# Optimization experiments

Hardware: AMD Instinct MI355X
Metric: run time of the kernel (lower is better)

## Reference

```python
import jax, jax.numpy as jnp
import numpy as np

N = 50000      # nodes
NE = 10000     # hyperedges
NNZ = 600000   # incidence pairs
DIN = 128
DOUT = 128
ALPHA_RES = 0.5  # module's residual mixing coefficient


def _glorot(key, shape):
    fan_in, fan_out = shape[1], shape[0]
    lim = float(np.sqrt(6.0 / (fan_in + fan_out)))
    return jax.random.uniform(key, shape, jnp.float32, -lim, lim)


def setup_inputs() -> dict:
    key = jax.random.key(0)
    ks = jax.random.split(key, 9)
    X = jax.random.normal(ks[0], (N, DIN), jnp.float32)
    X0 = jax.random.normal(ks[1], (N, DIN), jnp.float32)
    vertex = jax.random.randint(ks[2], (NNZ,), 0, N)
    edges = jax.random.randint(ks[3], (NNZ,), 0, NE)
    alpha = jax.random.uniform(ks[4], (NNZ,), jnp.float32)
    # single-layer MLPs -> plain Linear weights (out, in) + bias
    W1_w = _glorot(ks[5], (DOUT, DIN))
    W1_b = jnp.zeros((DOUT,), jnp.float32)
    W2_w = _glorot(ks[6], (DOUT, DIN + DOUT))
    W2_b = jnp.zeros((DOUT,), jnp.float32)
    W_w = _glorot(ks[7], (DOUT, DOUT))
    W_b = jnp.zeros((DOUT,), jnp.float32)
    return {"X": X, "vertex": vertex, "edges": edges, "X0": X0, "alpha": alpha,
            "W1_w": W1_w, "W1_b": W1_b, "W2_w": W2_w, "W2_b": W2_b,
            "W_w": W_w, "W_b": W_b}


def reference(X, vertex, edges, X0, alpha, W1_w, W1_b, W2_w, W2_b, W_w, W_b):
    a = alpha[:, None]                                   # [nnz,1]
    # vertex -> edge: gather W1(X) rows, weight, scatter-add over hyperedges
    Xw1 = X @ W1_w.T + W1_b                              # [N, dout]
    Xve = Xw1[vertex] * a                                # [nnz, dout]
    Xe = jax.ops.segment_sum(Xve, edges, num_segments=NE)  # [NE, dout]
    # edge -> vertex: gather edge feats, concat with raw vertex feats, W2, scatter-add
    Xev = jnp.concatenate([X[vertex], Xe[edges]], axis=-1)  # [nnz, din+dout]
    Xev = (Xev @ W2_w.T + W2_b) * a                      # [nnz, dout]
    Xv = jax.ops.segment_sum(Xev, vertex, num_segments=N)  # [N, dout]
    Xr = (1.0 - ALPHA_RES) * Xv + ALPHA_RES * X0         # residual mix
    return Xr @ W_w.T + W_b
```

## Files before the change

### kernel.cpp

```cpp
#include <hip/hip_runtime.h>

#define NV   50000
#define NEV  10000
#define NNZV 600000
#define DIM  128

#define NBKE 157
#define NBKV 196
#define CHUNK 4096
#define SCAP 7680

#define BPACK_OFF 0
#define WT1_OFF   24576
#define BA_OFF    40960
#define A_OFF     41216
#define B_OFF     91264
#define T_OFF     101312
#define XEBF_OFF  1381312
#define BCNTE_OFF 2021312
#define BOFFE_OFF 2021568
#define BCNTV_OFF 2021824
#define BOFFV_OFF 2022080
#define OFFE_OFF  2031328
#define CURE_OFF  2041344
#define OFFV_OFF  2101376
#define CURV_OFF  2151392
#define PV_OFF    2201920
#define PE_OUT_FLOAT_OFF 3200000

typedef __attribute__((ext_vector_type(8))) short bf16x8;
typedef __attribute__((ext_vector_type(4))) float f32x4;

__device__ __forceinline__ unsigned short f2bf(float x){
  unsigned u = __float_as_uint(x);
  u += 0x7fffu + ((u >> 16) & 1u);
  return (unsigned short)(u >> 16);
}
__device__ __forceinline__ float bf2f(unsigned short h){
  return __uint_as_float((unsigned)h << 16);
}

__global__ __launch_bounds__(128) void prep_weights(
        const float* __restrict__ W1w, const float* __restrict__ W2w,
        const float* __restrict__ W2b, const float* __restrict__ Ww,
        float* __restrict__ ws){
  int b = blockIdx.x, o = threadIdx.x;
  if (b < 384){
    float s;
    if (b < 256){
      float acc = 0.f;
      for (int m = 0; m < 128; ++m) acc += Ww[o*128 + m] * W2w[m*256 + b];
      s = 0.5f * acc;
    } else {
      s = 0.5f * Ww[o*128 + (b - 256)];
    }
    int ks = b >> 5, g = (b >> 3) & 3, j = b & 7;
    int ct = o >> 4, lo = o & 15;
    unsigned short* Bp = (unsigned short*)(ws + BPACK_OFF);
    Bp[((size_t)((ks*8 + ct)*64 + g*16 + lo))*8 + j] = f2bf(s);
  } else if (b < 512){
    int k = b - 384;
    ws[WT1_OFF + k*128 + o] = W1w[o*128 + k];
  } else {
    float acc = 0.f;
    for (int m = 0; m < 128; ++m) acc += Ww[o*128 + m] * W2b[m];
    ws[BA_OFF + o] = 0.5f * acc;
  }
}

__global__ __launch_bounds__(256) void count_bucket(
        const int* __restrict__ vertex, const int* __restrict__ edges,
        int* __restrict__ bcntE, int* __restrict__ bcntV){
  __shared__ int hE[256], hV[256];
  int t = threadIdx.x;
  hE[t] = 0; hV[t] = 0;
  __syncthreads();
  int i0 = blockIdx.x * 2048;
  #pragma unroll
  for (int r = 0; r < 8; ++r){
    int i = i0 + r*256 + t;
    if (i < NNZV){
      atomicAdd(&hE[edges[i]  >> 6], 1);
      atomicAdd(&hV[vertex[i] >> 8], 1);
    }
  }
  __syncthreads();
  if (hE[t]) atomicAdd(bcntE + t, hE[t]);
  if (hV[t]) atomicAdd(bcntV + t, hV[t]);
}

__global__ __launch_bounds__(256) void to_bf16(
        const float* __restrict__ src, unsigned short* __restrict__ dst, int n8){
  int i = blockIdx.x*256 + threadIdx.x;
  if (i >= n8) return;
  float4 v0 = ((const float4*)src)[(size_t)i*2];
  float4 v1 = ((const float4*)src)[(size_t)i*2 + 1];
  ushort4 h0, h1;
  h0.x=f2bf(v0.x); h0.y=f2bf(v0.y); h0.z=f2bf(v0.z); h0.w=f2bf(v0.w);
  h1.x=f2bf(v1.x); h1.y=f2bf(v1.y); h1.z=f2bf(v1.z); h1.w=f2bf(v1.w);
  ((ushort4*)dst)[(size_t)i*2]     = h0;
  ((ushort4*)dst)[(size_t)i*2 + 1] = h1;
}

__global__ __launch_bounds__(256) void scan_buckets(
        const int* __restrict__ bcntE, const int* __restrict__ bcntV,
        int* __restrict__ bOffE, int* __restrict__ bOffV,
        int* __restrict__ bcurE, int* __restrict__ bcurV,
        int* __restrict__ offE, int* __restrict__ offV){
  __shared__ int s[256];
  int t = threadIdx.x;
  int c = (t < NBKE) ? bcntE[t] : 0;
  s[t] = c; __syncthreads();
  for (int d = 1; d < 256; d <<= 1){
    int x = (t >= d) ? s[t-d] : 0;
    __syncthreads(); s[t] += x; __syncthreads();
  }
  if (t < NBKE){ bOffE[t] = s[t] - c; bcurE[t] = s[t] - c; }
  if (t == 0){ bOffE[NBKE] = NNZV; offE[NEV] = NNZV; }
  __syncthreads();
  int c2 = (t < NBKV) ? bcntV[t] : 0;
  s[t] = c2; __syncthreads();
  for (int d = 1; d < 256; d <<= 1){
    int x = (t >= d) ? s[t-d] : 0;
    __syncthreads(); s[t] += x; __syncthreads();
  }
  if (t < NBKV){ bOffV[t] = s[t] - c2; bcurV[t] = s[t] - c2; }
  if (t == 0){ bOffV[NBKV] = NNZV; offV[NV] = NNZV; }
}

__global__ __launch_bounds__(256) void fill_binned(
        const int* __restrict__ vertex, const int* __restrict__ edges,
        const float* __restrict__ alpha,
        int* __restrict__ bcur, int2* __restrict__ pairs,
        int isE, int nbk){
  __shared__ int hist[256], lofs[256], gbase[256], pos[256], ss[256];
  __shared__ int2 stage[CHUNK];
  int t = threadIdx.x;
  int i0 = blockIdx.x * CHUNK;
  if (t < nbk) hist[t] = 0;
  __syncthreads();
  int pk[16], pa[16], kb[16];
  #pragma unroll
  for (int r = 0; r < 16; ++r){
    int i = i0 + r*256 + t;
    int b = -1, packed = 0, ab = 0;
    if (i < NNZV){
      int v = vertex[i], e = edges[i];
      ab = __float_as_int(alpha[i]);
      packed = isE ? ((e << 16) | v) : ((v << 14) | e);
      b = packed >> 22;
      atomicAdd(&hist[b], 1);
    }
    pk[r] = packed; pa[r] = ab; kb[r] = b;
  }
  __syncthreads();
  int c = (t < nbk) ? hist[t] : 0;
  ss[t] = c; __syncthreads();
  for (int d = 1; d < 256; d <<= 1){
    int x = (t >= d) ? ss[t-d] : 0;
    __syncthreads(); ss[t] += x; __syncthreads();
  }
  if (t < nbk){ lofs[t] = ss[t] - c; pos[t] = ss[t] - c; }
  __syncthreads();
  #pragma unroll
  for (int r = 0; r < 16; ++r){
    if (kb[r] >= 0){
      int p = atomicAdd(&pos[kb[r]], 1);
      stage[p] = make_int2(pk[r], pa[r]);
    }
  }
  __syncthreads();
  if (t < nbk){
    int cnt = hist[t];
    gbase[t] = cnt ? atomicAdd(&bcur[t], cnt) : 0;
  }
  __syncthreads();
  int total = (i0 + CHUNK <= NNZV) ? CHUNK : (NNZV - i0);
  for (int s = t; s < total; s += 256){
    int lo = 0, hi = nbk - 1;
    while (lo < hi){ int mid = (lo + hi + 1) >> 1; if (lofs[mid] <= s) lo = mid; else hi = mid - 1; }
    pairs[gbase[lo] + (s - lofs[lo])] = stage[s];
  }
}

__global__ __launch_bounds__(256) void sort_bucket(
        int2* __restrict__ pairs, const int* __restrict__ bOff,
        int* __restrict__ off, int2* __restrict__ bounce,
        int kpb, int shift, int nkeys){
  int b = blockIdx.x, t = threadIdx.x;
  int k0 = b * kpb;
  int r0 = bOff[b], r1 = bOff[b+1];
  int m = r1 - r0;
  __shared__ int hist[256], rnk[256], ssc[256];
  __shared__ int2 srt[SCAP];
  for (int q = t; q < kpb; q += 256) hist[q] = 0;
  __syncthreads();
  int px[30], py[30];
  #pragma unroll
  for (int r = 0; r < 30; ++r){
    int s = r*256 + t;
    int x = -1, y = 0;
    if (s < m && m <= SCAP){
      int2 p = pairs[r0 + s];
      x = p.x; y = p.y;
      atomicAdd(&hist[(x >> shift) - k0], 1);
    }
    px[r] = x; py[r] = y;
  }
  if (m > SCAP){
    for (int s = t; s < m; s += 256){
      int2 p = pairs[r0 + s];
      bounce[s] = p;
      atomicAdd(&hist[(p.x >> shift) - k0], 1);
    }
  }
  __syncthreads();
  int c = (t < kpb) ? hist[t] : 0;
  ssc[t] = c; __syncthreads();
  for (int d = 1; d < 256; d <<= 1){
    int x = (t >= d) ? ssc[t-d] : 0;
    __syncthreads(); ssc[t] += x; __syncthreads();
  }
  if (t < kpb){
    rnk[t] = ssc[t] - c;
    int k = k0 + t;
    if (k < nkeys) off[k] = r0 + ssc[t] - c;
  }
  __syncthreads();
  if (m <= SCAP){
    #pragma unroll
    for (int r = 0; r < 30; ++r){
      if (px[r] >= 0){
        int p = atomicAdd(&rnk[(px[r] >> shift) - k0], 1);
        srt[p] = make_int2(px[r], py[r]);
      }
    }
    __syncthreads();
    for (int s = t; s < m; s += 256) pairs[r0 + s] = srt[s];
  } else {
    __syncthreads();
    for (int s = t; s < m; s += 256){
      int2 p = bounce[s];
      int q = atomicAdd(&rnk[(p.x >> shift) - k0], 1);
      pairs[r0 + q] = p;
    }
  }
}

__global__ __launch_bounds__(128) void edge_reduce(
        const unsigned short* __restrict__ Xbf, const int* __restrict__ offE,
        const int2* __restrict__ PE,
        float* __restrict__ T, float* __restrict__ B){
  int e = blockIdx.x, d = threadIdx.x;
  int s0 = offE[e], s1 = offE[e+1];
  __shared__ int   vs[128];
  __shared__ float as[128];
  float acc = 0.f, bacc = 0.f;
  for (int base = s0; base < s1; base += 128){
    int L = min(128, s1 - base);
    __syncthreads();
    if (d < L){
      int2 p = PE[base + d];
      vs[d] = p.x & 0xFFFF; as[d] = __int_as_float(p.y);
    }
    __syncthreads();
    for (int j = 0; j < L; ++j){
      float a = as[j];
      acc  += a * bf2f(Xbf[(size_t)vs[j]*DIM + d]);
      bacc += a;
    }
  }
  T[(size_t)e*DIM + d] = acc;
  if (d == 0) B[e] = bacc;
}

__global__ __launch_bounds__(256) void gemm_xe(const float* __restrict__ W1b,
                                               float* __restrict__ ws){
  __shared__ float Y[32][136];
  const float* T = ws + T_OFF;
  const float* Wt1 = ws + WT1_OFF;
  const float* Bs  = ws + B_OFF;
  unsigned short* Xe = (unsigned short*)(ws + XEBF_OFF);
  int n0 = blockIdx.x * 32;
  int tid = threadIdx.x;
  {
    int lr = tid >> 3, lj = tid & 7;
    int gn = n0 + lr; if (gn >= NEV) gn = NEV - 1;
    const float* src = T + (size_t)gn*DIM + lj*16;
    #pragma unroll
    for (int q = 0; q < 4; ++q)
      *(float4*)(&Y[lr][lj*16 + q*4]) = *(const float4*)(src + q*4);
  }
  __syncthreads();
  int rq = tid >> 5, cq = tid & 31;
  float acc[4][4];
  #pragma unroll
  for (int u=0;u<4;++u){ acc[u][0]=0;acc[u][1]=0;acc[u][2]=0;acc[u][3]=0; }
  const float* Crow = Wt1 + cq*4;
  #pragma unroll 4
  for (int k = 0; k < 128; ++k){
    float4 c = *(const float4*)(Crow + (size_t)k*128);
    #pragma unroll
    for (int u = 0; u < 4; ++u){
      float y = Y[rq*4 + u][k];
      acc[u][0] += y*c.x; acc[u][1] += y*c.y; acc[u][2] += y*c.z; acc[u][3] += y*c.w;
    }
  }
  float4 b1v = *(const float4*)(W1b + cq*4);
  #pragma unroll
  for (int u = 0; u < 4; ++u){
    int e = n0 + rq*4 + u;
    if (e < NEV){
      float Bv = Bs[e];
      ushort4 h;
      h.x = f2bf(acc[u][0] + Bv*b1v.x); h.y = f2bf(acc[u][1] + Bv*b1v.y);
      h.z = f2bf(acc[u][2] + Bv*b1v.z); h.w = f2bf(acc[u][3] + Bv*b1v.w);
      *(ushort4*)(Xe + (size_t)e*DIM + cq*4) = h;
    }
  }
}

__global__ __launch_bounds__(128) void vertex_reduce(
        const unsigned short* __restrict__ Xe, const int* __restrict__ offV,
        const int2* __restrict__ PV,
        float* __restrict__ S2, float* __restrict__ A){
  int v = blockIdx.x, d = threadIdx.x;
  int s0 = offV[v], s1 = offV[v+1];
  __shared__ int   es[128];
  __shared__ float as[128];
  float acc = 0.f, aacc = 0.f;
  for (int base = s0; base < s1; base += 128){
    int L = min(128, s1 - base);
    __syncthreads();
    if (d < L){
      int2 p = PV[base + d];
      es[d] = p.x & 0x3FFF; as[d] = __int_as_float(p.y);
    }
    __syncthreads();
    for (int j = 0; j < L; ++j){
      float a = as[j];
      acc  += a * bf2f(Xe[(size_t)es[j]*DIM + d]);
      aacc += a;
    }
  }
  S2[(size_t)v*DIM + d] = acc;
  if (d == 0) A[v] = aacc;
}

#define LDS_STRIDE 392

__global__ __launch_bounds__(256) void gemm_final_mfma(
        const float* __restrict__ X, const float* __restrict__ X0,
        const float* __restrict__ Wb, const float* __restrict__ ws,
        float* __restrict__ out){
  __shared__ unsigned short At[64 * LDS_STRIDE];
  __shared__ float ArS[64];
  const float* Aa = ws + A_OFF;
  const float* bA = ws + BA_OFF;
  const unsigned short* Bpack = (const unsigned short*)(ws + BPACK_OFF);
  int r0 = blockIdx.x * 64;
  int t = threadIdx.x;
  if (t < 64){
    int gn = r0 + t; if (gn >= NV) gn = NV - 1;
    ArS[t] = Aa[gn];
  }
  __syncthreads();
  #pragma unroll
  for (int seg = 0; seg < 3; ++seg){
    const float* src = (seg == 0) ? X : (seg == 1) ? out : X0;
    #pragma unroll
    for (int i = 0; i < 8; ++i){
      int idx = t + i*256;
      int row = idx >> 5;
      int c4  = idx & 31;
      int gn = r0 + row; if (gn >= NV) gn = NV - 1;
      float4 v = *(const float4*)(src + (size_t)gn*DIM + c4*4);
      if (seg == 0){
        float Ar = ArS[row];
        v.x *= Ar; v.y *= Ar; v.z *= Ar; v.w *= Ar;
      }
      ushort4 h;
      h.x = f2bf(v.x); h.y = f2bf(v.y); h.z = f2bf(v.z); h.w = f2bf(v.w);
      *(ushort4*)(&At[row*LDS_STRIDE + seg*128 + c4*4]) = h;
    }
  }
  __syncthreads();

  int w = t >> 6, l = t & 63;
  int m0 = w * 16;
  int lr = l & 15, lg = l >> 4;
  f32x4 acc[8];
  #pragma unroll
  for (int ct = 0; ct < 8; ++ct) acc[ct] = (f32x4){0.f,0.f,0.f,0.f};

  const unsigned short* arow = &At[(m0 + lr)*LDS_STRIDE + lg*8];
  for (int ks = 0; ks < 12; ++ks){
    bf16x8 af = *(const bf16x8*)(arow + ks*32);
    const bf16x8* bp = (const bf16x8*)(Bpack) + (size_t)ks*8*64 + l;
    #pragma unroll
    for (int ct = 0; ct < 8; ++ct){
      bf16x8 bf = bp[ct*64];
      acc[ct] = __builtin_amdgcn_mfma_f32_16x16x32_bf16(af, bf, acc[ct], 0, 0, 0);
    }
  }

  #pragma unroll
  for (int ct = 0; ct < 8; ++ct){
    int o = ct*16 + lr;
    float ba = bA[o], wb = Wb[o];
    #pragma unroll
    for (int r = 0; r < 4; ++r){
      int lrow = m0 + lg*4 + r;
      int row = r0 + lrow;
      if (row < NV){
        float Av = ArS[lrow];
        out[(size_t)row*DIM + o] = acc[ct][r] + Av*ba + wb;
      }
    }
  }
}

extern "C" void kernel_launch(void* const* d_in, const int* in_sizes, int n_in,
                              void* d_out, int out_size, void* d_ws, size_t ws_size,
                              hipStream_t stream){
  const float* X    = (const float*)d_in[0];
  const int*  vertex= (const int*)  d_in[1];
  const int*  edges = (const int*)  d_in[2];
  const float* X0   = (const float*)d_in[3];
  const float* alpha= (const float*)d_in[4];
  const float* W1w  = (const float*)d_in[5];
  const float* W1b  = (const float*)d_in[6];
  const float* W2w  = (const float*)d_in[7];
  const float* W2b  = (const float*)d_in[8];
  const float* Ww   = (const float*)d_in[9];
  const float* Wb   = (const float*)d_in[10];
  float* out = (float*)d_out;
  float* ws  = (float*)d_ws;

  int* bcntE = (int*)(ws + BCNTE_OFF);
  int* bOffE = (int*)(ws + BOFFE_OFF);
  int* bcntV = (int*)(ws + BCNTV_OFF);
  int* bOffV = (int*)(ws + BOFFV_OFF);
  int* offE  = (int*)(ws + OFFE_OFF);
  int* bcurE = (int*)(ws + CURE_OFF);
  int* offV  = (int*)(ws + OFFV_OFF);
  int* bcurV = (int*)(ws + CURV_OFF);
  int2* PV   = (int2*)(ws + PV_OFF);
  int2* PE   = (int2*)(out + PE_OUT_FLOAT_OFF);
  int2* bounce = (int2*)(ws + T_OFF);
  unsigned short* Xbf  = (unsigned short*)out;
  unsigned short* Xebf = (unsigned short*)(ws + XEBF_OFF);

  hipMemsetAsync(ws + BCNTE_OFF, 0, 1024u * 4, stream);

  prep_weights <<<513, 128, 0, stream>>>(W1w, W2w, W2b, Ww, ws);
  count_bucket <<<(NNZV + 2047)/2048, 256, 0, stream>>>(vertex, edges, bcntE, bcntV);
  to_bf16      <<<(NV*DIM/8 + 255)/256, 256, 0, stream>>>(X, Xbf, NV*DIM/8);
  scan_buckets <<<1, 256, 0, stream>>>(bcntE, bcntV, bOffE, bOffV, bcurE, bcurV, offE, offV);
  fill_binned  <<<(NNZV + CHUNK - 1)/CHUNK, 256, 0, stream>>>(vertex, edges, alpha,
                                                              bcurE, PE, 1, NBKE);
  fill_binned  <<<(NNZV + CHUNK - 1)/CHUNK, 256, 0, stream>>>(vertex, edges, alpha,
                                                              bcurV, PV, 0, NBKV);
  sort_bucket  <<<NBKE, 256, 0, stream>>>(PE, bOffE, offE, bounce, 64,  16, NEV);
  sort_bucket  <<<NBKV, 256, 0, stream>>>(PV, bOffV, offV, bounce, 256, 14, NV);
  edge_reduce  <<<NEV, 128, 0, stream>>>(Xbf, offE, PE, ws + T_OFF, ws + B_OFF);
  gemm_xe      <<<(NEV + 31)/32, 256, 0, stream>>>(W1b, ws);
  vertex_reduce<<<NV, 128, 0, stream>>>(Xebf, offV, PV, out, ws + A_OFF);
  gemm_final_mfma<<<(NV + 63)/64, 256, 0, stream>>>(X, X0, Wb, ws, out);
}
```

Before: 205.3 us.

## Fold final linear into edge features and fuse vertex reduce into output

Reassociates the math so the Xe half of W2 and the final W projection are premultiplied into a combined weight. The edge GEMM then directly produces per-edge output contributions (Ye), and the vertex reduction adds them straight into the output. The final MFMA GEMM shrinks its K from 384 to 256 (X and X0 only), and the per-segment alpha sums are computed inside sort_bucket. A kernel replaces the memset. The extra bf16 rounding of the premultiplied edge features and the changed summation order may shift numerics.

Result: no change. 203.7 us (-0.8%).

```diff
diff --git a/kernel.cpp b/kernel.cpp
--- a/kernel.cpp
+++ b/kernel.cpp
@@ -11,7 +11,7 @@
 #define SCAP 7680
 
 #define BPACK_OFF 0
-#define WT1_OFF   24576
+#define WP_OFF    24576
 #define BA_OFF    40960
 #define A_OFF     41216
 #define B_OFF     91264
@@ -40,31 +40,54 @@
   return __uint_as_float((unsigned)h << 16);
 }
 
-__global__ __launch_bounds__(128) void prep_weights(
-        const float* __restrict__ W1w, const float* __restrict__ W2w,
-        const float* __restrict__ W2b, const float* __restrict__ Ww,
-        float* __restrict__ ws){
+__global__ __launch_bounds__(256) void zero_counts(int* __restrict__ p){
+  int t = threadIdx.x;
+  #pragma unroll
+  for (int r = 0; r < 4; ++r) p[r*256 + t] = 0;
+}
+
+__global__ __launch_bounds__(128) void prep1(
+        const float* __restrict__ W2w, const float* __restrict__ W2b,
+        const float* __restrict__ Ww, float* __restrict__ ws){
   int b = blockIdx.x, o = threadIdx.x;
-  if (b < 384){
+  if (b < 256){
     float s;
-    if (b < 256){
+    if (b < 128){
       float acc = 0.f;
       for (int m = 0; m < 128; ++m) acc += Ww[o*128 + m] * W2w[m*256 + b];
       s = 0.5f * acc;
     } else {
-      s = 0.5f * Ww[o*128 + (b - 256)];
+      s = 0.5f * Ww[o*128 + (b - 128)];
     }
     int ks = b >> 5, g = (b >> 3) & 3, j = b & 7;
     int ct = o >> 4, lo = o & 15;
     unsigned short* Bp = (unsigned short*)(ws + BPACK_OFF);
     Bp[((size_t)((ks*8 + ct)*64 + g*16 + lo))*8 + j] = f2bf(s);
-  } else if (b < 512){
-    int k = b - 384;
-    ws[WT1_OFF + k*128 + o] = W1w[o*128 + k];
+  } else if (b < 384){
+    int m = b - 256;
+    float acc = 0.f;
+    for (int j = 0; j < 128; ++j) acc += Ww[o*128 + j] * W2w[j*256 + 128 + m];
+    ws[T_OFF + m*128 + o] = 0.5f * acc;
   } else {
     float acc = 0.f;
     for (int m = 0; m < 128; ++m) acc += Ww[o*128 + m] * W2b[m];
     ws[BA_OFF + o] = 0.5f * acc;
+  }
+}
+
+__global__ __launch_bounds__(128) void prep2(
+        const float* __restrict__ W1w, const float* __restrict__ W1b,
+        float* __restrict__ ws){
+  int b = blockIdx.x, o = threadIdx.x;
+  const float* C2t = ws + T_OFF;
+  if (b < 128){
+    float acc = 0.f;
+    for (int m = 0; m < 128; ++m) acc += W1w[m*128 + b] * C2t[m*128 + o];
+    ws[WP_OFF + b*128 + o] = acc;
+  } else {
+    float acc = 0.f;
+    for (int m = 0; m < 128; ++m) acc += W1b[m] * C2t[m*128 + o];
+    ws[BA_OFF + 128 + o] = acc;
   }
 }
 
@@ -185,8 +208,8 @@
 
 __global__ __launch_bounds__(256) void sort_bucket(
         int2* __restrict__ pairs, const int* __restrict__ bOff,
-        int* __restrict__ off, int2* __restrict__ bounce,
-        int kpb, int shift, int nkeys){
+        int* __restrict__ off, float* __restrict__ sums,
+        int2* __restrict__ bounce, int kpb, int shift, int nkeys){
   int b = blockIdx.x, t = threadIdx.x;
   int k0 = b * kpb;
   int r0 = bOff[b], r1 = bOff[b+1];
@@ -237,6 +260,15 @@
     }
     __syncthreads();
     for (int s = t; s < m; s += 256) pairs[r0 + s] = srt[s];
+    if (t < kpb){
+      int k = k0 + t;
+      if (k < nkeys){
+        float sa = 0.f;
+        int s0 = ssc[t] - hist[t], s1 = ssc[t];
+        for (int s = s0; s < s1; ++s) sa += __int_as_float(srt[s].y);
+        sums[k] = sa;
+      }
+    }
   } else {
     __syncthreads();
     for (int s = t; s < m; s += 256){
@@ -244,18 +276,27 @@
       int q = atomicAdd(&rnk[(p.x >> shift) - k0], 1);
       pairs[r0 + q] = p;
     }
+    __syncthreads();
+    if (t < kpb){
+      int k = k0 + t;
+      if (k < nkeys){
+        float sa = 0.f;
+        int s0 = ssc[t] - hist[t], s1 = ssc[t];
+        for (int s = s0; s < s1; ++s) sa += __int_as_float(pairs[r0 + s].y);
+        sums[k] = sa;
+      }
+    }
   }
 }
 
 __global__ __launch_bounds__(128) void edge_reduce(
         const unsigned short* __restrict__ Xbf, const int* __restrict__ offE,
-        const int2* __restrict__ PE,
-        float* __restrict__ T, float* __restrict__ B){
+        const int2* __restrict__ PE, float* __restrict__ T){
   int e = blockIdx.x, d = threadIdx.x;
   int s0 = offE[e], s1 = offE[e+1];
   __shared__ int   vs[128];
   __shared__ float as[128];
-  float acc = 0.f, bacc = 0.f;
+  float acc = 0.f;
   for (int base = s0; base < s1; base += 128){
     int L = min(128, s1 - base);
     __syncthreads();
@@ -264,23 +305,19 @@
       vs[d] = p.x & 0xFFFF; as[d] = __int_as_float(p.y);
     }
     __syncthreads();
-    for (int j = 0; j < L; ++j){
-      float a = as[j];
-      acc  += a * bf2f(Xbf[(size_t)vs[j]*DIM + d]);
-      bacc += a;
-    }
+    for (int j = 0; j < L; ++j)
+      acc += as[j] * bf2f(Xbf[(size_t)vs[j]*DIM + d]);
   }
   T[(size_t)e*DIM + d] = acc;
-  if (d == 0) B[e] = bacc;
-}
-
-__global__ __launch_bounds__(256) void gemm_xe(const float* __restrict__ W1b,
-                                               float* __restrict__ ws){
+}
+
+__global__ __launch_bounds__(256) void gemm_ye(float* __restrict__ ws){
   __shared__ float Y[32][136];
-  const float* T = ws + T_OFF;
-  const float* Wt1 = ws + WT1_OFF;
+  const float* T   = ws + T_OFF;
+  const float* WP  = ws + WP_OFF;
   const float* Bs  = ws + B_OFF;
-  unsigned short* Xe = (unsigned short*)(ws + XEBF_OFF);
+  const float* b1p = ws + BA_OFF + 128;
+  unsigned short* Ye = (unsigned short*)(ws + XEBF_OFF);
   int n0 = blockIdx.x * 32;
   int tid = threadIdx.x;
   {
@@ -296,7 +333,7 @@
   float acc[4][4];
   #pragma unroll
   for (int u=0;u<4;++u){ acc[u][0]=0;acc[u][1]=0;acc[u][2]=0;acc[u][3]=0; }
-  const float* Crow = Wt1 + cq*4;
+  const float* Crow = WP + cq*4;
   #pragma unroll 4
   for (int k = 0; k < 128; ++k){
     float4 c = *(const float4*)(Crow + (size_t)k*128);
@@ -306,7 +343,7 @@
       acc[u][0] += y*c.x; acc[u][1] += y*c.y; acc[u][2] += y*c.z; acc[u][3] += y*c.w;
     }
   }
-  float4 b1v = *(const float4*)(W1b + cq*4);
+  float4 b1v = *(const float4*)(b1p + cq*4);
   #pragma unroll
   for (int u = 0; u < 4; ++u){
     int e = n0 + rq*4 + u;
@@ -315,44 +352,17 @@
       ushort4 h;
       h.x = f2bf(acc[u][0] + Bv*b1v.x); h.y = f2bf(acc[u][1] + Bv*b1v.y);
       h.z = f2bf(acc[u][2] + Bv*b1v.z); h.w = f2bf(acc[u][3] + Bv*b1v.w);
-      *(ushort4*)(Xe + (size_t)e*DIM + cq*4) = h;
-    }
-  }
-}
-
-__global__ __launch_bounds__(128) void vertex_reduce(
-        const unsigned short* __restrict__ Xe, const int* __restrict__ offV,
-        const int2* __restrict__ PV,
-        float* __restrict__ S2, float* __restrict__ A){
-  int v = blockIdx.x, d = threadIdx.x;
-  int s0 = offV[v], s1 = offV[v+1];
-  __shared__ int   es[128];
-  __shared__ float as[128];
-  float acc = 0.f, aacc = 0.f;
-  for (int base = s0; base < s1; base += 128){
-    int L = min(128, s1 - base);
-    __syncthreads();
-    if (d < L){
-      int2 p = PV[base + d];
-      es[d] = p.x & 0x3FFF; as[d] = __int_as_float(p.y);
-    }
-    __syncthreads();
-    for (int j = 0; j < L; ++j){
-      float a = as[j];
-      acc  += a * bf2f(Xe[(size_t)es[j]*DIM + d]);
-      aacc += a;
-    }
-  }
-  S2[(size_t)v*DIM + d] = acc;
-  if (d == 0) A[v] = aacc;
-}
-
-#define LDS_STRIDE 392
-
-__global__ __launch_bounds__(256) void gemm_final_mfma(
+      *(ushort4*)(Ye + (size_t)e*DIM + cq*4) = h;
+    }
+  }
+}
+
+#define LDS_STRIDE 264
+
+__global__ __launch_bounds__(256) void gemm_pq(
         const float* __restrict__ X, const float* __restrict__ X0,
         const float* __restrict__ Wb, const float* __restrict__ ws,
-        float* __restrict__ out){
+        float* __restrict__ R){
   __shared__ unsigned short At[64 * LDS_STRIDE];
   __shared__ float ArS[64];
   const float* Aa = ws + A_OFF;
@@ -366,8 +376,8 @@
   }
   __syncthreads();
   #pragma unroll
-  for (int seg = 0; seg < 3; ++seg){
-    const float* src = (seg == 0) ? X : (seg == 1) ? out : X0;
+  for (int seg = 0; seg < 2; ++seg){
+    const float* src = (seg == 0) ? X : X0;
     #pragma unroll
     for (int i = 0; i < 8; ++i){
       int idx = t + i*256;
@@ -394,7 +404,8 @@
   for (int ct = 0; ct < 8; ++ct) acc[ct] = (f32x4){0.f,0.f,0.f,0.f};
 
   const unsigned short* arow = &At[(m0 + lr)*LDS_STRIDE + lg*8];
-  for (int ks = 0; ks < 12; ++ks){
+  #pragma unroll
+  for (int ks = 0; ks < 8; ++ks){
     bf16x8 af = *(const bf16x8*)(arow + ks*32);
     const bf16x8* bp = (const bf16x8*)(Bpack) + (size_t)ks*8*64 + l;
     #pragma unroll
@@ -414,10 +425,32 @@
       int row = r0 + lrow;
       if (row < NV){
         float Av = ArS[lrow];
-        out[(size_t)row*DIM + o] = acc[ct][r] + Av*ba + wb;
+        R[(size_t)row*DIM + o] = acc[ct][r] + Av*ba + wb;
       }
     }
   }
+}
+
+__global__ __launch_bounds__(128) void vertex_fused(
+        const unsigned short* __restrict__ Ye, const int* __restrict__ offV,
+        const int2* __restrict__ PV, float* __restrict__ out){
+  int v = blockIdx.x, d = threadIdx.x;
+  int s0 = offV[v], s1 = offV[v+1];
+  __shared__ int   es[128];
+  __shared__ float as[128];
+  float acc = 0.f;
+  for (int base = s0; base < s1; base += 128){
+    int L = min(128, s1 - base);
+    __syncthreads();
+    if (d < L){
+      int2 p = PV[base + d];
+      es[d] = p.x & 0x3FFF; as[d] = __int_as_float(p.y);
+    }
+    __syncthreads();
+    for (int j = 0; j < L; ++j)
+      acc += as[j] * bf2f(Ye[(size_t)es[j]*DIM + d]);
+  }
+  out[(size_t)v*DIM + d] += acc;
 }
 
 extern "C" void kernel_launch(void* const* d_in, const int* in_sizes, int n_in,
@@ -448,12 +481,12 @@
   int2* PV   = (int2*)(ws + PV_OFF);
   int2* PE   = (int2*)(out + PE_OUT_FLOAT_OFF);
   int2* bounce = (int2*)(ws + T_OFF);
-  unsigned short* Xbf  = (unsigned short*)out;
-  unsigned short* Xebf = (unsigned short*)(ws + XEBF_OFF);
-
-  hipMemsetAsync(ws + BCNTE_OFF, 0, 1024u * 4, stream);
-
-  prep_weights <<<513, 128, 0, stream>>>(W1w, W2w, W2b, Ww, ws);
+  unsigned short* Xbf = (unsigned short*)out;
+  unsigned short* Ye  = (unsigned short*)(ws + XEBF_OFF);
+
+  zero_counts  <<<1, 256, 0, stream>>>(bcntE);
+  prep1        <<<385, 128, 0, stream>>>(W2w, W2b, Ww, ws);
+  prep2        <<<129, 128, 0, stream>>>(W1w, W1b, ws);
   count_bucket <<<(NNZV + 2047)/2048, 256, 0, stream>>>(vertex, edges, bcntE, bcntV);
   to_bf16      <<<(NV*DIM/8 + 255)/256, 256, 0, stream>>>(X, Xbf, NV*DIM/8);
   scan_buckets <<<1, 256, 0, stream>>>(bcntE, bcntV, bOffE, bOffV, bcurE, bcurV, offE, offV);
@@ -461,10 +494,10 @@
                                                               bcurE, PE, 1, NBKE);
   fill_binned  <<<(NNZV + CHUNK - 1)/CHUNK, 256, 0, stream>>>(vertex, edges, alpha,
                                                               bcurV, PV, 0, NBKV);
-  sort_bucket  <<<NBKE, 256, 0, stream>>>(PE, bOffE, offE, bounce, 64,  16, NEV);
-  sort_bucket  <<<NBKV, 256, 0, stream>>>(PV, bOffV, offV, bounce, 256, 14, NV);
-  edge_reduce  <<<NEV, 128, 0, stream>>>(Xbf, offE, PE, ws + T_OFF, ws + B_OFF);
-  gemm_xe      <<<(NEV + 31)/32, 256, 0, stream>>>(W1b, ws);
-  vertex_reduce<<<NV, 128, 0, stream>>>(Xebf, offV, PV, out, ws + A_OFF);
-  gemm_final_mfma<<<(NV + 63)/64, 256, 0, stream>>>(X, X0, Wb, ws, out);
-}
+  sort_bucket  <<<NBKE, 256, 0, stream>>>(PE, bOffE, offE, ws + B_OFF, bounce, 64,  16, NEV);
+  sort_bucket  <<<NBKV, 256, 0, stream>>>(PV, bOffV, offV, ws + A_OFF, bounce, 256, 14, NV);
+  edge_reduce  <<<NEV, 128, 0, stream>>>(Xbf, offE, PE, ws + T_OFF);
+  gemm_ye      <<<(NEV + 31)/32, 256, 0, stream>>>(ws);
+  gemm_pq      <<<(NV + 63)/64, 256, 0, stream>>>(X, X0, Wb, ws, out);
+  vertex_fused <<<NV, 128, 0, stream>>>(Ye, offV, PV, out);
+}
```
